# Kernel optimization log

Measured on AMD Instinct MI355X. Metric: run time of the kernel, lower is better.

Reference implementation:

```python
import jax, jax.numpy as jnp
import numpy as np

EPS = 1e-5

def mean_variance_norm(x):
    # x: [b,c,h,w]; torch .var(dim=2) on flattened spatial is UNBIASED (n-1)
    b, c, h, w = x.shape
    n = h * w
    mean = jnp.mean(x, axis=(2, 3), keepdims=True)
    var = jnp.sum((x - mean) ** 2, axis=(2, 3), keepdims=True) / (n - 1) + EPS
    return (x - mean) / jnp.sqrt(var)

def conv1x1(x, W, b):
    # 1x1 conv == channel-mixing matmul. W: [out_c, in_c], b: [out_c]
    return jnp.einsum('oc,bchw->bohw', W, x) + b[None, :, None, None]

def setup_inputs() -> dict:
    key = jax.random.key(0)
    ks = jax.random.split(key, 10)
    C = 512
    shp = (4, C, 64, 64)
    std = 1.0 / np.sqrt(C)
    return {
        'content': jax.random.normal(ks[0], shp, jnp.float32),
        'style': jax.random.normal(ks[1], shp, jnp.float32),
        'Wf': jax.random.normal(ks[2], (C, C), jnp.float32) * std,
        'bf': jax.random.normal(ks[3], (C,), jnp.float32) * 0.01,
        'Wg': jax.random.normal(ks[4], (C, C), jnp.float32) * std,
        'bg': jax.random.normal(ks[5], (C,), jnp.float32) * 0.01,
        'Wh': jax.random.normal(ks[6], (C, C), jnp.float32) * std,
        'bh': jax.random.normal(ks[7], (C,), jnp.float32) * 0.01,
        'Wo': jax.random.normal(ks[8], (C, C), jnp.float32) * std,
        'bo': jax.random.normal(ks[9], (C,), jnp.float32) * 0.01,
    }

def reference(content, style, Wf, bf, Wg, bg, Wh, bh, Wo, bo):
    b, c, h, w = content.shape
    hw = h * w
    F = conv1x1(mean_variance_norm(content), Wf, bf).reshape(b, c, hw)  # queries
    G = conv1x1(mean_variance_norm(style), Wg, bg).reshape(b, c, hw)    # keys
    H = conv1x1(style, Wh, bh).reshape(b, c, hw)                        # values
    # S[b,n,m] = sum_c F[b,c,n] * G[b,c,m]  (unscaled attention scores)
    S = jnp.einsum('bcn,bcm->bnm', F, G)
    S = jax.nn.softmax(S, axis=-1)
    # O[b,c,n] = sum_m H[b,c,m] * S[b,n,m]
    O = jnp.einsum('bcm,bnm->bcn', H, S).reshape(b, c, h, w)
    O = conv1x1(O, Wo, bo)
    return O + content
```

## Files before the change

### kernel.cpp

```cpp
#include <hip/hip_runtime.h>

#define C 512
#define HW 4096
#define EPSV 1e-5f

typedef _Float16 fp16x8 __attribute__((ext_vector_type(8)));
typedef _Float16 fp16x4 __attribute__((ext_vector_type(4)));
typedef float f32x4 __attribute__((ext_vector_type(4)));

#define OFF_MC    (0)
#define OFF_RC    (8192)
#define OFF_MS    (16384)
#define OFF_RS    (24576)
#define OFF_BETAF (32768)
#define OFF_V     (40960)
#define OFF_BZ    (49152)
#define OFF_T     (65536)
#define OFF_SP    (131072)
#define OFF_A     (OFF_SP + 2097152)
#define OFF_WZ    (OFF_A + 1048576)
#define OFF_XCT   (OFF_WZ + 1048576)
#define OFF_XST   (OFF_XCT + 16777216)
#define OFF_KT    (OFF_XST + 16777216)
#define OFF_HM    (OFF_KT + 16777216)
#define OFF_ML    (OFF_HM + 16777216)
#define OFF_S     (OFF_ML + 8388608)

#define FT_IDX(n, c) ((((size_t)((n) >> 4) * 16 + ((c) >> 5)) * 512) + \
                      ((((c) >> 3) & 3) * 128) + (((n) & 15) * 8) + ((c) & 7))


__global__ void transpose_stats_kernel(const float* __restrict__ xc, const float* __restrict__ xs,
                                       char* __restrict__ ws)
{
    int bx = blockIdx.x;
    int tensor = bx >> 11, b = (bx >> 9) & 3, c0 = ((bx >> 6) & 7) * 64, n0 = (bx & 63) * 64;
    const float* src = tensor ? xs : xc;
    _Float16* dst = (_Float16*)(ws + (tensor ? OFF_XST : OFF_XCT));
    float2* part = (float2*)(ws + OFF_SP);

    __shared__ _Float16 tile[64][72];
    __shared__ float sred[4][64], ssred[4][64];

    int tid = threadIdx.x, cR = tid & 63, ng = tid >> 6;
    const float* p = src + ((size_t)(b * C + c0 + cR)) * HW + n0 + ng * 16;
    float s = 0.f, ss = 0.f;
    #pragma unroll
    for (int k = 0; k < 4; k++) {
        float4 v = *(const float4*)(p + k * 4);
        s += v.x + v.y + v.z + v.w;
        ss += v.x * v.x + v.y * v.y + v.z * v.z + v.w * v.w;
        int n = ng * 16 + k * 4;
        tile[n][cR] = (_Float16)v.x; tile[n + 1][cR] = (_Float16)v.y;
        tile[n + 2][cR] = (_Float16)v.z; tile[n + 3][cR] = (_Float16)v.w;
    }
    sred[ng][cR] = s; ssred[ng][cR] = ss;
    __syncthreads();
    if (tid < 64) {
        float S = sred[0][tid] + sred[1][tid] + sred[2][tid] + sred[3][tid];
        float SS = ssred[0][tid] + ssred[1][tid] + ssred[2][tid] + ssred[3][tid];
        part[((size_t)((tensor * 4 + b) * 512 + c0 + tid)) * 64 + (n0 >> 6)] = make_float2(S, SS);
    }
    _Float16* dstB = dst + (size_t)b * HW * C;
    #pragma unroll
    for (int i = 0; i < 2; i++) {
        int g = tid + i * 256, row = g >> 3, c8 = (g & 7) * 8;
        int n = n0 + row, c = c0 + c8;
        *(fp16x8*)&dstB[FT_IDX(n, c)] = *(const fp16x8*)&tile[row][c8];
    }
}

__global__ void finalize_stats_kernel(char* __restrict__ ws)
{
    int ch = blockIdx.x * 256 + threadIdx.x;
    const float2* part = (const float2*)(ws + OFF_SP) + (size_t)ch * 64;
    float S = 0.f, SS = 0.f;
    for (int k = 0; k < 64; k++) { float2 v = part[k]; S += v.x; SS += v.y; }
    int tensor = ch >> 11, rem = ch & 2047;
    float m = S / (float)HW;
    float var = (SS - S * m) / (float)(HW - 1) + EPSV;
    ((float*)(ws + (tensor ? OFF_MS : OFF_MC)))[rem] = m;
    ((float*)(ws + (tensor ? OFF_RS : OFF_RC)))[rem] = rsqrtf(var);
}

__global__ void precompute_kernel(const float* __restrict__ Wf, const float* __restrict__ Wg,
                                  const float* __restrict__ Wo, const float* __restrict__ Wh,
                                  const float* __restrict__ bf, const float* __restrict__ bh,
                                  char* __restrict__ ws)
{
    float* A = (float*)(ws + OFF_A);
    float* Wz = (float*)(ws + OFF_WZ);
    float* betaf = (float*)(ws + OFF_BETAF);
    float* bz = (float*)(ws + OFF_BZ);
    const float* mc = (const float*)(ws + OFF_MC);
    const float* rc = (const float*)(ws + OFF_RC);
    int bx = blockIdx.x, t = threadIdx.x;
    if (bx < 512) {
        bool isA = bx < 256;
        int r0 = (isA ? bx : bx - 256) * 2;
        float a00 = 0.f, a01 = 0.f, a10 = 0.f, a11 = 0.f;
        for (int k = 0; k < C; k++) {
            float r0v, r1v, c0v, c1v;
            if (isA) {
                r0v = Wf[k * C + r0]; r1v = Wf[k * C + r0 + 1];
                c0v = Wg[k * C + t];  c1v = Wg[k * C + t + 256];
            } else {
                r0v = Wo[r0 * C + k]; r1v = Wo[(r0 + 1) * C + k];
                c0v = Wh[k * C + t];  c1v = Wh[k * C + t + 256];
            }
            a00 += r0v * c0v; a01 += r0v * c1v;
            a10 += r1v * c0v; a11 += r1v * c1v;
        }
        float* D = isA ? A : Wz;
        D[r0 * C + t] = a00;       D[r0 * C + t + 256] = a01;
        D[(r0 + 1) * C + t] = a10; D[(r0 + 1) * C + t + 256] = a11;
    } else if (bx < 520) {
        int g = (bx - 512) * 256 + t, b = g >> 9, co = g & 511;
        float acc = 0.f;
        for (int i = 0; i < C; i++) acc += Wf[co * C + i] * mc[b * C + i] * rc[b * C + i];
        betaf[g] = bf[co] - acc;
    } else {
        int co = (bx - 520) * 256 + t;
        float acc = 0.f;
        for (int i = 0; i < C; i++) acc += Wo[co * C + i] * bh[i];
        bz[co] = acc;
    }
}

__global__ void precompute_v_kernel(const float* __restrict__ Wg, char* __restrict__ ws)
{
    const float* betaf = (const float*)(ws + OFF_BETAF);
    const float* rs = (const float*)(ws + OFF_RS);
    float* v = (float*)(ws + OFF_V);
    int g = blockIdx.x * 32 + (threadIdx.x >> 3);
    int b = g >> 9, j = g & 511, cq = threadIdx.x & 7;
    float acc = 0.f;
    for (int co = cq * 64; co < cq * 64 + 64; co++) acc += betaf[b * C + co] * Wg[co * C + j];
    acc += __shfl_xor(acc, 1);
    acc += __shfl_xor(acc, 2);
    acc += __shfl_xor(acc, 4);
    if (cq == 0) v[g] = rs[b * C + j] * acc;
}

__global__ void __launch_bounds__(256) prep_gemm_kernel(char* __restrict__ ws)
{
    const float* A = (const float*)(ws + OFF_A);
    const float* Wz = (const float*)(ws + OFF_WZ);
    const float* rc = (const float*)(ws + OFF_RC);
    const float* rs = (const float*)(ws + OFF_RS);
    const float* bz = (const float*)(ws + OFF_BZ);
    const _Float16* __restrict__ xsT = (const _Float16*)(ws + OFF_XST);
    _Float16* __restrict__ Kt = (_Float16*)(ws + OFF_KT);
    _Float16* __restrict__ Hp = (_Float16*)(ws + OFF_HM);

    int bx = blockIdx.x;
    int b = bx & 3, rest = bx >> 2;
    int r128 = rest >> 5, mb = rest & 31;
    int r0 = r128 * 128, m0 = mb * 128;
    int w = threadIdx.x >> 6, lane = threadIdx.x & 63, q = lane >> 4, l16 = lane & 15;
    int wr = (w & 1) * 64, wm = (w >> 1) * 64;
    bool isK = (r0 < 512);
    const float* Asrc = isK ? A : Wz;
    int rbase = (isK ? r0 : r0 - 512) + wr;

    f32x4 zz = {0.f, 0.f, 0.f, 0.f};
    f32x4 acc[4][4];
    #pragma unroll
    for (int rt = 0; rt < 4; rt++)
        #pragma unroll
        for (int mt = 0; mt < 4; mt++) acc[rt][mt] = zz;

    float rcv[4];
    #pragma unroll
    for (int rt = 0; rt < 4; rt++)
        rcv[rt] = isK ? rc[b * C + rbase + rt * 16 + l16] : 1.f;

    const _Float16* xb = xsT + (size_t)b * HW * C
                             + (size_t)((m0 + wm) >> 4) * 8192 + q * 128 + l16 * 8;

    for (int ks = 0; ks < 16; ks++) {
        int j0 = ks * 32 + q * 8;
        float rsv[8];
        if (isK) {
            float4 u0 = *(const float4*)&rs[b * C + j0];
            float4 u1 = *(const float4*)&rs[b * C + j0 + 4];
            rsv[0] = u0.x; rsv[1] = u0.y; rsv[2] = u0.z; rsv[3] = u0.w;
            rsv[4] = u1.x; rsv[5] = u1.y; rsv[6] = u1.z; rsv[7] = u1.w;
        } else {
            #pragma unroll
            for (int jj = 0; jj < 8; jj++) rsv[jj] = 1.f;
        }
        fp16x8 afr[4];
        #pragma unroll
        for (int rt = 0; rt < 4; rt++) {
            int row = rbase + rt * 16 + l16;
            float4 a0 = *(const float4*)&Asrc[row * C + j0];
            float4 a1 = *(const float4*)&Asrc[row * C + j0 + 4];
            float av8[8];
            av8[0] = a0.x; av8[1] = a0.y; av8[2] = a0.z; av8[3] = a0.w;
            av8[4] = a1.x; av8[5] = a1.y; av8[6] = a1.z; av8[7] = a1.w;
            float sc = rcv[rt];
            #pragma unroll
            for (int jj = 0; jj < 8; jj++)
                afr[rt][jj] = (_Float16)(isK ? av8[jj] * sc * rsv[jj] : av8[jj]);
        }
        fp16x8 bfr[4];
        #pragma unroll
        for (int mt = 0; mt < 4; mt++)
            bfr[mt] = *(const fp16x8*)(xb + (size_t)(mt * 16 + ks) * 512);
        #pragma unroll
        for (int rt = 0; rt < 4; rt++)
            #pragma unroll
            for (int mt = 0; mt < 4; mt++)
                acc[rt][mt] = __builtin_amdgcn_mfma_f32_16x16x32_f16(afr[rt], bfr[mt], acc[rt][mt], 0, 0, 0);
    }

    if (isK) {
        _Float16* KtB = Kt + (size_t)b * HW * C;
        #pragma unroll
        for (int rt = 0; rt < 4; rt++)
            #pragma unroll
            for (int mt = 0; mt < 4; mt++) {
                int m = m0 + wm + mt * 16 + l16;
                int cb = r0 + wr + rt * 16 + q * 4;
                fp16x4 h;
                h[0] = (_Float16)acc[rt][mt][0]; h[1] = (_Float16)acc[rt][mt][1];
                h[2] = (_Float16)acc[rt][mt][2]; h[3] = (_Float16)acc[rt][mt][3];
                *(fp16x4*)&KtB[FT_IDX(m, cb)] = h;
            }
    } else {
        _Float16* HpB = Hp + (size_t)b * 2097152;
        #pragma unroll
        for (int rt = 0; rt < 4; rt++) {
            float bzv[4];
            #pragma unroll
            for (int reg = 0; reg < 4; reg++) bzv[reg] = bz[rbase + rt * 16 + q * 4 + reg];
            #pragma unroll
            for (int mt = 0; mt < 4; mt++) {
                int m = m0 + wm + mt * 16 + l16;
                int mbase = (m >> 3) * 128 + (m & 7);
                #pragma unroll
                for (int reg = 0; reg < 4; reg++) {
                    int co = rbase + rt * 16 + q * 4 + reg;
                    HpB[(size_t)(co >> 4) * 65536 + mbase + (co & 15) * 8] =
                        (_Float16)(acc[rt][mt][reg] + bzv[reg]);
                }
            }
        }
    }
}

__global__ void t_kernel(char* __restrict__ ws)
{
    const float* v = (const float*)(ws + OFF_V);
    const _Float16* __restrict__ xsT = (const _Float16*)(ws + OFF_XST);
    float* tG = (float*)(ws + OFF_T);
    int bx = blockIdx.x;
    int b = bx >> 7, m0 = (bx & 127) * 32;
    int m = m0 + (threadIdx.x >> 3), cq = threadIdx.x & 7;
    const _Float16* p = xsT + (size_t)b * HW * C + (size_t)(m >> 4) * 8192 + (m & 15) * 8;
    const float* vp = v + b * C + cq * 64;
    float acc = 0.f;
    #pragma unroll
    for (int k = 0; k < 8; k++) {
        fp16x8 xv = *(const fp16x8*)(p + (cq * 2 + (k >> 2)) * 512 + (k & 3) * 128);
        float4 v0 = *(const float4*)(vp + k * 8);
        float4 v1 = *(const float4*)(vp + k * 8 + 4);
        acc += (float)xv[0] * v0.x + (float)xv[1] * v0.y + (float)xv[2] * v0.z + (float)xv[3] * v0.w
             + (float)xv[4] * v1.x + (float)xv[5] * v1.y + (float)xv[6] * v1.z + (float)xv[7] * v1.w;
    }
    acc += __shfl_xor(acc, 1);
    acc += __shfl_xor(acc, 2);
    acc += __shfl_xor(acc, 4);
    if (cq == 0) tG[b * HW + m] = acc;
}

__global__ void __launch_bounds__(256, 4) qk_kernel(char* __restrict__ ws)
{
    const _Float16* __restrict__ xcT = (const _Float16*)(ws + OFF_XCT);
    const _Float16* __restrict__ Kt = (const _Float16*)(ws + OFF_KT);
    const float* __restrict__ tG = (const float*)(ws + OFF_T);
    float2* __restrict__ ML = (float2*)(ws + OFF_ML);
    _Float16* __restrict__ Sg = (_Float16*)(ws + OFF_S);

    int bx = blockIdx.x;
    int b = (bx >> 1) & 3, mhi = bx & 1;
    int rest = bx >> 3, mlo = rest & 15, ntile = rest >> 4;
    int m0 = (mhi * 16 + mlo) * 128, n0 = ntile * 128;
    int tid = threadIdx.x, w = tid >> 6, lane = tid & 63, q = lane >> 4, l16 = lane & 15;
    int wn = (w & 1) * 64, wm = (w >> 1) * 64;

    const _Float16* ab = xcT + (size_t)b * HW * C
                             + (size_t)((n0 + wn) >> 4) * 8192 + q * 128 + l16 * 8;
    const _Float16* bb = Kt + (size_t)b * HW * C
                            + (size_t)((m0 + wm) >> 4) * 8192 + q * 128 + l16 * 8;

    f32x4 zz = {0.f, 0.f, 0.f, 0.f};
    f32x4 acc[4][4];
    #pragma unroll
    for (int nt = 0; nt < 4; nt++)
        #pragma unroll
        for (int mt = 0; mt < 4; mt++) acc[nt][mt] = zz;

    #pragma unroll 4
    for (int ks = 0; ks < 16; ks++) {
        fp16x8 afr[4], bfr[4];
        #pragma unroll
        for (int nt = 0; nt < 4; nt++)
            afr[nt] = *(const fp16x8*)(ab + (size_t)(nt * 16 + ks) * 512);
        #pragma unroll
        for (int mt = 0; mt < 4; mt++)
            bfr[mt] = *(const fp16x8*)(bb + (size_t)(mt * 16 + ks) * 512);
        #pragma unroll
        for (int nt = 0; nt < 4; nt++)
            #pragma unroll
            for (int mt = 0; mt < 4; mt++)
                acc[nt][mt] = __builtin_amdgcn_mfma_f32_16x16x32_f16(afr[nt], bfr[mt], acc[nt][mt], 0, 0, 0);
    }

    float tv[4];
    #pragma unroll
    for (int mt = 0; mt < 4; mt++) tv[mt] = tG[b * HW + m0 + wm + mt * 16 + l16];
    #pragma unroll
    for (int nt = 0; nt < 4; nt++)
        #pragma unroll
        for (int mt = 0; mt < 4; mt++)
            #pragma unroll
            for (int reg = 0; reg < 4; reg++) acc[nt][mt][reg] += tv[mt];

    float rm[4][4], sum[4][4];
    #pragma unroll
    for (int nt = 0; nt < 4; nt++)
        #pragma unroll
        for (int reg = 0; reg < 4; reg++)
            rm[nt][reg] = fmaxf(fmaxf(acc[nt][0][reg], acc[nt][1][reg]),
                                fmaxf(acc[nt][2][reg], acc[nt][3][reg]));
    #pragma unroll
    for (int s = 1; s < 16; s <<= 1)
        #pragma unroll
        for (int nt = 0; nt < 4; nt++)
            #pragma unroll
            for (int reg = 0; reg < 4; reg++)
                rm[nt][reg] = fmaxf(rm[nt][reg], __shfl_xor(rm[nt][reg], s));
    #pragma unroll
    for (int nt = 0; nt < 4; nt++)
        #pragma unroll
        for (int reg = 0; reg < 4; reg++) sum[nt][reg] = 0.f;
    #pragma unroll
    for (int nt = 0; nt < 4; nt++)
        #pragma unroll
        for (int mt = 0; mt < 4; mt++)
            #pragma unroll
            for (int reg = 0; reg < 4; reg++) {
                float pv = __expf(acc[nt][mt][reg] - rm[nt][reg]);
                acc[nt][mt][reg] = pv;
                sum[nt][reg] += pv;
            }
    #pragma unroll
    for (int s = 1; s < 16; s <<= 1)
        #pragma unroll
        for (int nt = 0; nt < 4; nt++)
            #pragma unroll
            for (int reg = 0; reg < 4; reg++)
                sum[nt][reg] += __shfl_xor(sum[nt][reg], s);

    int tl = (m0 + wm) >> 6;
    if (l16 == 0) {
        #pragma unroll
        for (int nt = 0; nt < 4; nt++)
            #pragma unroll
            for (int reg = 0; reg < 4; reg++)
                ML[((size_t)(b * HW + n0 + wn + nt * 16 + q * 4 + reg)) * 64 + tl] =
                    make_float2(rm[nt][reg], sum[nt][reg]);
    }

    __shared__ _Float16 Pl[4][64][72];
    #pragma unroll
    for (int nt = 0; nt < 4; nt++)
        #pragma unroll
        for (int mt = 0; mt < 4; mt++)
            #pragma unroll
            for (int reg = 0; reg < 4; reg++)
                Pl[w][nt * 16 + q * 4 + reg][mt * 16 + l16] = (_Float16)acc[nt][mt][reg];
    __syncthreads();
    #pragma unroll
    for (int i = 0; i < 8; i++) {
        int row = i * 8 + (lane >> 3), c8 = (lane & 7) * 8;
        *(fp16x8*)&Sg[((size_t)(b * HW + n0 + wn + row)) * HW + m0 + wm + c8] =
            *(const fp16x8*)&Pl[w][row][c8];
    }
}

__global__ void __launch_bounds__(512, 4) pv_kernel(const float* __restrict__ xc,
                                                    const float* __restrict__ bo,
                                                    float* __restrict__ out,
                                                    char* __restrict__ ws)
{
    const _Float16* __restrict__ Sg = (const _Float16*)(ws + OFF_S);
    const _Float16* __restrict__ Hp = (const _Float16*)(ws + OFF_HM);
    const float2* __restrict__ ML = (const float2*)(ws + OFF_ML);

    int bx = blockIdx.x;
    int b = bx & 3, cohalf = (bx >> 2) & 1, ntile = bx >> 3;
    int n0 = ntile * 64, co0 = cohalf * 256;
    int tid = threadIdx.x, w = tid >> 6, lane = tid & 63, q = lane >> 4, l16 = lane & 15;
    int wn = (w & 1) * 32, wc = (w >> 1) * 64;

    __shared__ _Float16 SclH[64][72];
    __shared__ _Float16 Al[2][64][72];

    {
        int row = tid >> 3, g = tid & 7;
        const float2* mlp = ML + ((size_t)(b * HW + n0 + row)) * 64 + g * 8;
        float2 v[8];
        #pragma unroll
        for (int k = 0; k < 8; k++) v[k] = mlp[k];
        float M = v[0].x;
        #pragma unroll
        for (int k = 1; k < 8; k++) M = fmaxf(M, v[k].x);
        M = fmaxf(M, __shfl_xor(M, 1));
        M = fmaxf(M, __shfl_xor(M, 2));
        M = fmaxf(M, __shfl_xor(M, 4));
        float e[8], L = 0.f;
        #pragma unroll
        for (int k = 0; k < 8; k++) { e[k] = __expf(v[k].x - M); L += v[k].y * e[k]; }
        L += __shfl_xor(L, 1);
        L += __shfl_xor(L, 2);
        L += __shfl_xor(L, 4);
        float linv = 1.f / L;
        #pragma unroll
        for (int k = 0; k < 8; k++) SclH[g * 8 + k][row] = (_Float16)(e[k] * linv);
    }

    int sr = tid >> 3, sc16 = tid & 7;
    const _Float16* sp = Sg + ((size_t)(b * HW + n0 + sr)) * HW + sc16 * 8;
    {
        fp16x8 st = *(const fp16x8*)(sp);
        *(fp16x8*)&Al[0][sr][sc16 * 8] = st;
    }

    f32x4 zz = {0.f, 0.f, 0.f, 0.f};
    f32x4 acc[2][4];
    #pragma unroll
    for (int nt = 0; nt < 2; nt++)
        #pragma unroll
        for (int ct = 0; ct < 4; ct++) acc[nt][ct] = zz;

    const _Float16* hb = Hp + (size_t)b * 2097152
                            + (size_t)((co0 + wc) >> 4) * 65536
                            + (size_t)q * 128 + (size_t)l16 * 8;

    for (int chunk = 0; chunk < 64; chunk++) {
        int buf = chunk & 1;
        __syncthreads();
        fp16x8 st;
        if (chunk < 63) st = *(const fp16x8*)(sp + (chunk + 1) * 64);

        fp16x8 bfr[2][4];
        #pragma unroll
        for (int km = 0; km < 2; km++)
            #pragma unroll
            for (int ct = 0; ct < 4; ct++)
                bfr[km][ct] = *(const fp16x8*)(hb + (size_t)ct * 65536 + (chunk * 8 + km * 4) * 128);

        f32x4 tmp[2][4];
        #pragma unroll
        for (int km = 0; km < 2; km++) {
            int k = km * 32 + q * 8;
            fp16x8 afr[2];
            #pragma unroll
            for (int nt = 0; nt < 2; nt++)
                afr[nt] = *(const fp16x8*)&Al[buf][wn + nt * 16 + l16][k];
            #pragma unroll
            for (int nt = 0; nt < 2; nt++)
                #pragma unroll
                for (int ct = 0; ct < 4; ct++)
                    tmp[nt][ct] = __builtin_amdgcn_mfma_f32_16x16x32_f16(
                        afr[nt], bfr[km][ct], km == 0 ? zz : tmp[nt][ct], 0, 0, 0);
        }
        #pragma unroll
        for (int nt = 0; nt < 2; nt++) {
            fp16x4 svh = *(const fp16x4*)&SclH[chunk][wn + nt * 16 + q * 4];
            float sv[4];
            #pragma unroll
            for (int reg = 0; reg < 4; reg++) sv[reg] = (float)svh[reg];
            #pragma unroll
            for (int ct = 0; ct < 4; ct++)
                #pragma unroll
                for (int reg = 0; reg < 4; reg++)
                    acc[nt][ct][reg] += tmp[nt][ct][reg] * sv[reg];
        }
        if (chunk < 63) {
            *(fp16x8*)&Al[buf ^ 1][sr][sc16 * 8] = st;
        }
    }

    #pragma unroll
    for (int nt = 0; nt < 2; nt++)
        #pragma unroll
        for (int ct = 0; ct < 4; ct++) {
            int co = co0 + wc + ct * 16 + l16;
            size_t base = ((size_t)(b * C + co)) * HW + n0 + wn + nt * 16 + q * 4;
            float4 cv = *(const float4*)&xc[base];
            float bov = bo[co];
            float4 o;
            o.x = acc[nt][ct][0] + bov + cv.x;
            o.y = acc[nt][ct][1] + bov + cv.y;
            o.z = acc[nt][ct][2] + bov + cv.z;
            o.w = acc[nt][ct][3] + bov + cv.w;
            *(float4*)&out[base] = o;
        }
}

extern "C" void kernel_launch(void* const* d_in, const int* in_sizes, int n_in,
                              void* d_out, int out_size, void* d_ws, size_t ws_size,
                              hipStream_t stream)
{
    const float* content = (const float*)d_in[0];
    const float* style   = (const float*)d_in[1];
    const float* Wf = (const float*)d_in[2];
    const float* bf = (const float*)d_in[3];
    const float* Wg = (const float*)d_in[4];
    const float* Wh = (const float*)d_in[6];
    const float* bh = (const float*)d_in[7];
    const float* Wo = (const float*)d_in[8];
    const float* bo = (const float*)d_in[9];
    float* out = (float*)d_out;
    char* ws = (char*)d_ws;

    transpose_stats_kernel<<<4096, 256, 0, stream>>>(content, style, ws);
    finalize_stats_kernel<<<16, 256, 0, stream>>>(ws);
    precompute_kernel<<<522, 256, 0, stream>>>(Wf, Wg, Wo, Wh, bf, bh, ws);
    precompute_v_kernel<<<64, 256, 0, stream>>>(Wg, ws);
    prep_gemm_kernel<<<1024, 256, 0, stream>>>(ws);
    t_kernel<<<512, 256, 0, stream>>>(ws);
    qk_kernel<<<4096, 256, 0, stream>>>(ws);
    pv_kernel<<<512, 512, 0, stream>>>(content, bo, out, ws);
}
```

Measured before the change: 512.3 us.

## Store scores in MFMA fragment layout and read PV operands directly from global

The QK kernel now writes the fp16 score matrix in a fragment-tiled layout, so the PV kernel can load MFMA A-operands straight from global memory. This removes the LDS staging, double buffering and per-chunk barriers. Softmax rescale factors are now computed once by a separate scale_kernel into a transposed fp32 buffer, instead of being recomputed in every PV block. Each PV block now covers 32 rows and all 512 output channels rather than 64 rows and half the channels, which trades more global traffic per block for no synchronisation and fewer redundant score reads.

After: 550.9 us. 1.08x slower.

```diff
diff --git a/kernel.cpp b/kernel.cpp
--- a/kernel.cpp
+++ b/kernel.cpp
@@ -28,6 +28,9 @@
 
 #define FT_IDX(n, c) ((((size_t)((n) >> 4) * 16 + ((c) >> 5)) * 512) + \
                       ((((c) >> 3) & 3) * 128) + (((n) & 15) * 8) + ((c) & 7))
+
+#define SFT_IDX(n, m) ((((size_t)((n) >> 4) * 128 + ((m) >> 5)) * 512) + \
+                       ((((m) >> 3) & 3) * 128) + (((n) & 15) * 8) + ((m) & 7))
 
 
 __global__ void transpose_stats_kernel(const float* __restrict__ xc, const float* __restrict__ xs,
@@ -383,61 +386,65 @@
             for (int reg = 0; reg < 4; reg++)
                 Pl[w][nt * 16 + q * 4 + reg][mt * 16 + l16] = (_Float16)acc[nt][mt][reg];
     __syncthreads();
+    _Float16* SgB = Sg + (size_t)b * 16777216;
     #pragma unroll
     for (int i = 0; i < 8; i++) {
         int row = i * 8 + (lane >> 3), c8 = (lane & 7) * 8;
-        *(fp16x8*)&Sg[((size_t)(b * HW + n0 + wn + row)) * HW + m0 + wm + c8] =
-            *(const fp16x8*)&Pl[w][row][c8];
-    }
-}
-
-__global__ void __launch_bounds__(512, 4) pv_kernel(const float* __restrict__ xc,
-                                                    const float* __restrict__ bo,
-                                                    float* __restrict__ out,
-                                                    char* __restrict__ ws)
-{
-    const _Float16* __restrict__ Sg = (const _Float16*)(ws + OFF_S);
+        int n = n0 + wn + row, m = m0 + wm + c8;
+        *(fp16x8*)&SgB[SFT_IDX(n, m)] = *(const fp16x8*)&Pl[w][row][c8];
+    }
+}
+
+__global__ void scale_kernel(char* __restrict__ ws)
+{
+    const float2* __restrict__ ML = (const float2*)(ws + OFF_ML);
+    float* __restrict__ Scl = (float*)(ws + OFF_XCT);
+    int g = blockIdx.x * 128 + threadIdx.x;
+    const float2* mlp = ML + (size_t)g * 64;
+    float M = -1e30f;
+    #pragma unroll
+    for (int k = 0; k < 64; k += 4) {
+        float4 a = *(const float4*)(mlp + k);
+        float4 c = *(const float4*)(mlp + k + 2);
+        M = fmaxf(M, fmaxf(fmaxf(a.x, a.z), fmaxf(c.x, c.z)));
+    }
+    float L = 0.f;
+    #pragma unroll
+    for (int k = 0; k < 64; k += 2) {
+        float4 a = *(const float4*)(mlp + k);
+        L += a.y * __expf(a.x - M) + a.w * __expf(a.z - M);
+    }
+    float linv = 1.f / L;
+    int b = g >> 12, n = g & 4095;
+    float* sp = Scl + (size_t)b * 262144 + n;
+    #pragma unroll
+    for (int k = 0; k < 64; k += 2) {
+        float4 a = *(const float4*)(mlp + k);
+        sp[(size_t)k * 4096] = __expf(a.x - M) * linv;
+        sp[(size_t)(k + 1) * 4096] = __expf(a.z - M) * linv;
+    }
+}
+
+__global__ void __launch_bounds__(512) pv_kernel(const float* __restrict__ xc,
+                                                 const float* __restrict__ bo,
+                                                 float* __restrict__ out,
+                                                 char* __restrict__ ws)
+{
+    const _Float16* __restrict__ Sft = (const _Float16*)(ws + OFF_S);
     const _Float16* __restrict__ Hp = (const _Float16*)(ws + OFF_HM);
-    const float2* __restrict__ ML = (const float2*)(ws + OFF_ML);
+    const float* __restrict__ Scl = (const float*)(ws + OFF_XCT);
 
     int bx = blockIdx.x;
-    int b = bx & 3, cohalf = (bx >> 2) & 1, ntile = bx >> 3;
-    int n0 = ntile * 64, co0 = cohalf * 256;
+    int b = bx & 3, ntile = bx >> 2;
+    int n0 = ntile * 32;
     int tid = threadIdx.x, w = tid >> 6, lane = tid & 63, q = lane >> 4, l16 = lane & 15;
-    int wn = (w & 1) * 32, wc = (w >> 1) * 64;
-
-    __shared__ _Float16 SclH[64][72];
-    __shared__ _Float16 Al[2][64][72];
-
-    {
-        int row = tid >> 3, g = tid & 7;
-        const float2* mlp = ML + ((size_t)(b * HW + n0 + row)) * 64 + g * 8;
-        float2 v[8];
-        #pragma unroll
-        for (int k = 0; k < 8; k++) v[k] = mlp[k];
-        float M = v[0].x;
-        #pragma unroll
-        for (int k = 1; k < 8; k++) M = fmaxf(M, v[k].x);
-        M = fmaxf(M, __shfl_xor(M, 1));
-        M = fmaxf(M, __shfl_xor(M, 2));
-        M = fmaxf(M, __shfl_xor(M, 4));
-        float e[8], L = 0.f;
-        #pragma unroll
-        for (int k = 0; k < 8; k++) { e[k] = __expf(v[k].x - M); L += v[k].y * e[k]; }
-        L += __shfl_xor(L, 1);
-        L += __shfl_xor(L, 2);
-        L += __shfl_xor(L, 4);
-        float linv = 1.f / L;
-        #pragma unroll
-        for (int k = 0; k < 8; k++) SclH[g * 8 + k][row] = (_Float16)(e[k] * linv);
-    }
-
-    int sr = tid >> 3, sc16 = tid & 7;
-    const _Float16* sp = Sg + ((size_t)(b * HW + n0 + sr)) * HW + sc16 * 8;
-    {
-        fp16x8 st = *(const fp16x8*)(sp);
-        *(fp16x8*)&Al[0][sr][sc16 * 8] = st;
-    }
+    int co0 = w * 64;
+
+    const _Float16* sb = Sft + (size_t)b * 16777216
+                             + (size_t)(ntile * 2) * 65536 + q * 128 + l16 * 8;
+    const _Float16* hb = Hp + (size_t)b * 2097152 + (size_t)(co0 >> 4) * 65536
+                            + q * 128 + l16 * 8;
+    const float* sc = Scl + (size_t)b * 262144 + n0 + q * 4;
 
     f32x4 zz = {0.f, 0.f, 0.f, 0.f};
     f32x4 acc[2][4];
@@ -446,61 +453,46 @@
         #pragma unroll
         for (int ct = 0; ct < 4; ct++) acc[nt][ct] = zz;
 
-    const _Float16* hb = Hp + (size_t)b * 2097152
-                            + (size_t)((co0 + wc) >> 4) * 65536
-                            + (size_t)q * 128 + (size_t)l16 * 8;
-
     for (int chunk = 0; chunk < 64; chunk++) {
-        int buf = chunk & 1;
-        __syncthreads();
-        fp16x8 st;
-        if (chunk < 63) st = *(const fp16x8*)(sp + (chunk + 1) * 64);
-
-        fp16x8 bfr[2][4];
-        #pragma unroll
-        for (int km = 0; km < 2; km++)
+        fp16x8 afr[2][2], bfr[2][4];
+        #pragma unroll
+        for (int km = 0; km < 2; km++) {
+            #pragma unroll
+            for (int nt = 0; nt < 2; nt++)
+                afr[km][nt] = *(const fp16x8*)(sb + (size_t)nt * 65536 + (chunk * 2 + km) * 512);
             #pragma unroll
             for (int ct = 0; ct < 4; ct++)
                 bfr[km][ct] = *(const fp16x8*)(hb + (size_t)ct * 65536 + (chunk * 8 + km * 4) * 128);
+        }
+        float4 sv0 = *(const float4*)(sc + chunk * 4096);
+        float4 sv1 = *(const float4*)(sc + chunk * 4096 + 16);
 
         f32x4 tmp[2][4];
         #pragma unroll
-        for (int km = 0; km < 2; km++) {
-            int k = km * 32 + q * 8;
-            fp16x8 afr[2];
-            #pragma unroll
-            for (int nt = 0; nt < 2; nt++)
-                afr[nt] = *(const fp16x8*)&Al[buf][wn + nt * 16 + l16][k];
+        for (int km = 0; km < 2; km++)
             #pragma unroll
             for (int nt = 0; nt < 2; nt++)
                 #pragma unroll
                 for (int ct = 0; ct < 4; ct++)
                     tmp[nt][ct] = __builtin_amdgcn_mfma_f32_16x16x32_f16(
-                        afr[nt], bfr[km][ct], km == 0 ? zz : tmp[nt][ct], 0, 0, 0);
-        }
-        #pragma unroll
-        for (int nt = 0; nt < 2; nt++) {
-            fp16x4 svh = *(const fp16x4*)&SclH[chunk][wn + nt * 16 + q * 4];
-            float sv[4];
-            #pragma unroll
-            for (int reg = 0; reg < 4; reg++) sv[reg] = (float)svh[reg];
+                        afr[km][nt], bfr[km][ct], km == 0 ? zz : tmp[nt][ct], 0, 0, 0);
+
+        float sva[2][4] = {{sv0.x, sv0.y, sv0.z, sv0.w}, {sv1.x, sv1.y, sv1.z, sv1.w}};
+        #pragma unroll
+        for (int nt = 0; nt < 2; nt++)
             #pragma unroll
             for (int ct = 0; ct < 4; ct++)
                 #pragma unroll
                 for (int reg = 0; reg < 4; reg++)
-                    acc[nt][ct][reg] += tmp[nt][ct][reg] * sv[reg];
-        }
-        if (chunk < 63) {
-            *(fp16x8*)&Al[buf ^ 1][sr][sc16 * 8] = st;
-        }
+                    acc[nt][ct][reg] += tmp[nt][ct][reg] * sva[nt][reg];
     }
 
     #pragma unroll
     for (int nt = 0; nt < 2; nt++)
         #pragma unroll
         for (int ct = 0; ct < 4; ct++) {
-            int co = co0 + wc + ct * 16 + l16;
-            size_t base = ((size_t)(b * C + co)) * HW + n0 + wn + nt * 16 + q * 4;
+            int co = co0 + ct * 16 + l16;
+            size_t base = ((size_t)(b * C + co)) * HW + n0 + nt * 16 + q * 4;
             float4 cv = *(const float4*)&xc[base];
             float bov = bo[co];
             float4 o;
@@ -535,5 +527,6 @@
     prep_gemm_kernel<<<1024, 256, 0, stream>>>(ws);
     t_kernel<<<512, 256, 0, stream>>>(ws);
     qk_kernel<<<4096, 256, 0, stream>>>(ws);
+    scale_kernel<<<128, 128, 0, stream>>>(ws);
     pv_kernel<<<512, 512, 0, stream>>>(content, bo, out, ws);
 }
```
